# Performance work log

Measured on AMD Instinct MI355X. Metric: run time of the kernel, lower is better.

## Reference

```python
import jax, jax.numpy as jnp
import numpy as np

N = 32768       # batch of states
DQ = 8          # q_ndim (dof_ndim)
A = 4           # action_dim
H = 1024        # hidden_size


def setup_inputs() -> dict:
    key = jax.random.key(0)
    ks = jax.random.split(key, 16)

    def lin(kw, kb, fan_out, fan_in, zero_bias=False):
        s = 1.0 / np.sqrt(fan_in)
        W = jax.random.normal(kw, (fan_out, fan_in), dtype=jnp.float32) * s
        b = jnp.zeros((fan_out,), jnp.float32) if zero_bias else \
            jax.random.normal(kb, (fan_out,), dtype=jnp.float32) * s
        return W, b

    W1, b1 = lin(ks[0], ks[1], H, 2 * DQ)            # h_net layer 1
    W2, b2 = lin(ks[2], ks[3], H, H)                 # h_net layer 2
    Wh, bh = lin(ks[4], ks[5], 1, H)                 # h_net head -> scalar H(z)
    Wf1, bf1 = lin(ks[6], ks[7], H, 2 * DQ + A)      # flex_net layer 1
    Wf2, bf2 = lin(ks[8], ks[9], H, H)               # flex_net layer 2
    Wff, bff = lin(ks[10], ks[11], 2 * DQ, H)        # flex_net head -> 2*q_ndim
    Wp, bp = lin(ks[12], ks[13], A, 2 * DQ)          # control policy (detached)

    return {
        "t": jnp.zeros((), jnp.float32),
        "z": jax.random.normal(ks[14], (N, 2 * DQ), dtype=jnp.float32),
        "W1": W1, "b1": b1, "W2": W2, "b2": b2, "Wh": Wh, "bh": bh,
        "Wf1": Wf1, "bf1": bf1, "Wf2": Wf2, "bf2": bf2, "Wff": Wff, "bff": bff,
        "Wp": Wp, "bp": bp,
    }


def reference(t, z, W1, b1, W2, b2, Wh, bh,
              Wf1, bf1, Wf2, bf2, Wff, bff, Wp, bp):
    # control input, detached as in the torch forward (u = policy(t, z).detach())
    u = jax.lax.stop_gradient(jnp.tanh(z @ Wp.T + bp))  # [N, A]

    # ---- H-net forward, saving tanh' at each activation (the `sps` list) ----
    # angular_dims=() -> CosSin is the identity, so h_net[0](z) = z.
    a1 = z @ W1.T + b1          # [N, H]
    h1 = jnp.tanh(a1)
    s0 = 1.0 - h1 * h1          # d tanh / d a1   (sps[0])
    a2 = h1 @ W2.T + b2         # [N, H]
    h2 = jnp.tanh(a2)
    s1 = 1.0 - h2 * h2          # d tanh / d a2   (sps[1])

    # dH = grad_z sum(h_net(z)), with gradients flowing (create_graph=True)
    def H_sum(zz):
        hh = jnp.tanh(zz @ W1.T + b1)
        hh = jnp.tanh(hh @ W2.T + b2)
        return jnp.sum(hh @ Wh.T + bh)

    dH = jax.grad(H_sum)(z)     # [N, 2*DQ]

    # ---- flex-net with skip term modulated by reversed tanh' maps ----
    zu = jnp.concatenate([z, u], axis=-1)       # [N, 2*DQ + A]
    f1 = zu @ Wf1.T + bf1
    g1 = jnp.tanh(f1) + f1 * s1                 # idx = 1 -> sps[1]
    f2 = g1 @ Wf2.T + bf2
    g2 = jnp.tanh(f2) + f2 * s0                 # idx = 0 -> sps[0]
    out = g2 @ Wff.T + bff                      # [N, 2*DQ]

    # D = jacobian of CosSin = identity per batch row (angular_dims=()), so
    # bmm(out[:,None,:], D).squeeze(1) == out.

    # dz_dt = J @ (out + dH):  J([top; bot]) = [bot; -top]
    s = out + dH
    return jnp.concatenate([s[:, DQ:], -s[:, :DQ]], axis=-1)  # [N, 2*DQ]
```

## Files before the change

kernel.cpp:

```cpp
#include <hip/hip_runtime.h>
#include <hip/hip_bf16.h>

typedef __hip_bfloat16 bf16;
typedef __attribute__((ext_vector_type(8))) short short8;
typedef __attribute__((ext_vector_type(4))) short s16x4;
typedef __attribute__((ext_vector_type(4))) float f32x4;

__device__ __forceinline__ bf16 f2b(float f) { return __float2bfloat16(f); }
__device__ __forceinline__ short bfbits(float f) {
  union { float f; unsigned u; } x; x.f = f;
  unsigned r = x.u + 0x7fff + ((x.u >> 16) & 1);
  return (short)(r >> 16);
}
__device__ __forceinline__ float tanh_fast(float x) {
  float t = __expf(-2.f * fabsf(x));
  float r = (1.f - t) * __builtin_amdgcn_rcpf(1.f + t);
  return copysignf(r, x);
}

#define GLOAD_LDS16(gp, lp) __builtin_amdgcn_global_load_lds( \
    (const __attribute__((address_space(1))) void*)(gp), \
    (__attribute__((address_space(3))) void*)(lp), 16, 0, 0)
#define SBAR() __builtin_amdgcn_s_barrier()
#define WAITV(n) do { asm volatile("s_waitcnt vmcnt(" #n ")" ::: "memory"); \
                      __builtin_amdgcn_sched_barrier(0); } while (0)

__global__ __launch_bounds__(256) void prep(
    const float* __restrict__ W2, const float* __restrict__ Wf2,
    const float* __restrict__ W1, const float* __restrict__ Wff,
    bf16* __restrict__ W2bf, bf16* __restrict__ W2Tbf,
    bf16* __restrict__ Wf2bf, bf16* __restrict__ W1n,
    bf16* __restrict__ Wffn)
{
  __shared__ float T[32][33];
  const int tid = threadIdx.x, bx = blockIdx.x;
  const int tx = bx & 31, ty = bx >> 5;
  const int r = tid >> 3, c4 = (tid & 7) * 4;
  const long ibase = (long)(ty * 32 + r) * 1024 + tx * 32 + c4;

  f32x4 v = *(const f32x4*)(W2 + ibase);
  f32x4 vf = *(const f32x4*)(Wf2 + ibase);
  s16x4 sv, sf;
  #pragma unroll
  for (int j = 0; j < 4; ++j) {
    sv[j] = bfbits(v[j]); sf[j] = bfbits(vf[j]);
    T[r][c4 + j] = v[j];
  }
  *(s16x4*)(W2bf + ibase) = sv;
  *(s16x4*)(Wf2bf + ibase) = sf;
  __syncthreads();
  const int oc = tid >> 3, or4 = (tid & 7) * 4;
  s16x4 st;
  #pragma unroll
  for (int j = 0; j < 4; ++j) st[j] = bfbits(T[or4 + j][oc]);
  *(s16x4*)(W2Tbf + (long)(tx * 32 + oc) * 1024 + ty * 32 + or4) = st;

  if (bx < 32) {
    #pragma unroll
    for (int rep = 0; rep < 2; ++rep) {
      int i = bx * 512 + rep * 256 + tid;
      int rr = i >> 10, cc = i & 1023;
      W1n[i] = f2b(W1[cc * 16 + rr]);
      Wffn[i] = f2b(Wff[i]);
    }
  }
}

__global__ __launch_bounds__(256) void k1(
    const float* __restrict__ z, const float* __restrict__ W1,
    const float* __restrict__ b1, const float* __restrict__ Wp,
    const float* __restrict__ bp, const float* __restrict__ Wf1,
    const float* __restrict__ bf1v,
    bf16* __restrict__ h1, bf16* __restrict__ f1out, long grow0)
{
  __shared__ float zs[32][16];
  __shared__ float us[32][4];
  const int tid = threadIdx.x;
  const long r0 = (long)blockIdx.x * 32;
  for (int i = tid; i < 512; i += 256) {
    int r = i >> 4, c = i & 15;
    zs[r][c] = z[(grow0 + r0 + r) * 16 + c];
  }
  __syncthreads();
  if (tid < 128) {
    int r = tid >> 2, a = tid & 3;
    float acc = bp[a];
    #pragma unroll
    for (int k = 0; k < 16; ++k) acc = fmaf(zs[r][k], Wp[a * 16 + k], acc);
    us[r][a] = tanh_fast(acc);
  }
  __syncthreads();
  #pragma unroll
  for (int jj = 0; jj < 4; ++jj) {
    const int c = tid + jj * 256;
    {
      float w[16];
      #pragma unroll
      for (int k = 0; k < 16; ++k) w[k] = W1[c * 16 + k];
      const float bc = b1[c];
      for (int r = 0; r < 32; ++r) {
        float a = bc;
        #pragma unroll
        for (int k = 0; k < 16; ++k) a = fmaf(zs[r][k], w[k], a);
        h1[(r0 + r) * 1024 + c] = f2b(tanh_fast(a));
      }
    }
    {
      float wf[20];
      #pragma unroll
      for (int k = 0; k < 20; ++k) wf[k] = Wf1[c * 20 + k];
      const float bfc = bf1v[c];
      for (int r = 0; r < 32; ++r) {
        float f = bfc;
        #pragma unroll
        for (int k = 0; k < 16; ++k) f = fmaf(zs[r][k], wf[k], f);
        #pragma unroll
        for (int a = 0; a < 4; ++a) f = fmaf(us[r][a], wf[16 + a], f);
        f1out[(r0 + r) * 1024 + c] = f2b(f);
      }
    }
  }
}

__global__ __launch_bounds__(512, 2) void gemm0(
    const bf16* __restrict__ A, const bf16* __restrict__ Bp,
    const float* __restrict__ bias, const float* __restrict__ Whv,
    bf16* O1, bf16* __restrict__ O2)
{
  __shared__ __align__(16) char smem[131072];
  const int tid = threadIdx.x;
  const int lane = tid & 63, wid = tid >> 6;
  const int wr = wid >> 2, wc = wid & 3;
  const int fr = lane & 15, kg = lane >> 4;
  const long row0 = (long)blockIdx.x * 256;
  const int col0 = blockIdx.y * 256;

  const int sr0 = tid >> 2;
  const int sk0 = ((tid & 3) ^ ((tid >> 3) & 3)) * 8;
  const int swr = (fr >> 1) & 3;

  const bf16* gA0 = A + (row0 + sr0) * 1024 + sk0;
  const bf16* gB0 = Bp + ((long)col0 + sr0) * 1024 + sk0;
  const int rdA = (wr * 128 + fr) * 32 + (kg ^ swr) * 8;
  const int rdB = (wc * 64 + fr) * 32 + (kg ^ swr) * 8;

  f32x4 acc[8][4] = {};

  auto stage = [&](int b, int k0) {
    bf16* as = (bf16*)smem + b * 8192;
    bf16* bs = (bf16*)smem + 32768 + b * 8192;
    GLOAD_LDS16(gA0 + k0, as + tid * 8);
    GLOAD_LDS16(gA0 + 128 * 1024 + k0, as + 4096 + tid * 8);
    GLOAD_LDS16(gB0 + k0, bs + tid * 8);
    GLOAD_LDS16(gB0 + 128 * 1024 + k0, bs + 4096 + tid * 8);
  };

  stage(0, 0); stage(1, 32); stage(2, 64);
  WAITV(8); SBAR();

  #pragma unroll
  for (int kt = 0; kt < 32; ++kt) {
    if (kt + 3 < 32) stage((kt + 3) & 3, (kt + 3) * 32);
    const bf16* as = (const bf16*)smem + (kt & 3) * 8192;
    const bf16* bs = (const bf16*)smem + 32768 + (kt & 3) * 8192;
    short8 af[8], bfr[4];
    #pragma unroll
    for (int m = 0; m < 8; ++m)
      af[m] = *(const short8*)(as + rdA + m * 512);
    #pragma unroll
    for (int n = 0; n < 4; ++n)
      bfr[n] = *(const short8*)(bs + rdB + n * 512);
    __builtin_amdgcn_s_setprio(1);
    #pragma unroll
    for (int m = 0; m < 8; ++m)
      #pragma unroll
      for (int n = 0; n < 4; ++n)
        acc[m][n] = __builtin_amdgcn_mfma_f32_16x16x32_bf16(af[m], bfr[n], acc[m][n], 0, 0, 0);
    __builtin_amdgcn_s_setprio(0);
    if (kt < 29)       WAITV(8);
    else if (kt == 29) WAITV(4);
    else if (kt == 30) WAITV(0);
    if (kt < 31) SBAR();
  }

  #pragma unroll
  for (int m = 0; m < 8; ++m) {
    const long gr0 = row0 + wr * 128 + m * 16 + kg * 4;
    #pragma unroll
    for (int n = 0; n < 4; ++n) {
      const int gc = col0 + wc * 64 + n * 16 + fr;
      const float b2c = bias[gc], whc = Whv[gc];
      f32x4 v = acc[m][n];
      #pragma unroll
      for (int j = 0; j < 4; ++j) {
        const long idx = (gr0 + j) * 1024 + gc;
        float h = tanh_fast(v[j] + b2c);
        float s1v = 1.f - h * h;
        float f = __bfloat162float(((const bf16*)O1)[idx]);
        O2[idx] = f2b(s1v * whc);
        O1[idx] = f2b(tanh_fast(f) + f * s1v);
      }
    }
  }
}

__global__ __launch_bounds__(256, 2) void gemm12(
    const bf16* __restrict__ Ab, const bf16* __restrict__ Af,
    const bf16* __restrict__ Bw, const bf16* __restrict__ Bf,
    const float* __restrict__ bf2v, const bf16* __restrict__ h1,
    const bf16* __restrict__ W1n, const bf16* __restrict__ Wffn,
    float* __restrict__ Pp, int ckRows)
{
  __shared__ __align__(16) char smem[65536];
  const int tid = threadIdx.x;
  const int lane = tid & 63, wid = tid >> 6;
  const int wr = wid >> 1, wc = wid & 1;
  const int fr = lane & 15, kg = lane >> 4;

  const int q = (int)gridDim.x >> 3;
  const int wgid = ((int)blockIdx.x & 7) * q + ((int)blockIdx.x >> 3);
  const long row0 = (long)(wgid >> 3) * 128;
  const int col0 = (wgid & 7) * 128;
  const int cb = wgid & 7;

  const int sr0 = tid >> 2;
  const int sk0 = ((tid & 3) ^ ((tid >> 3) & 3)) * 8;
  const int swr = (fr >> 1) & 3;

  const bf16* gAb = Ab + (row0 + sr0) * 1024 + sk0;
  const bf16* gAf = Af + (row0 + sr0) * 1024 + sk0;
  const bf16* gBw = Bw + ((long)col0 + sr0) * 1024 + sk0;
  const bf16* gBf = Bf + ((long)col0 + sr0) * 1024 + sk0;
  const int rdA = (wr * 64 + fr) * 32 + (kg ^ swr) * 8;
  const int rdB = (wc * 64 + fr) * 32 + (kg ^ swr) * 8;

  f32x4 accB[4][4] = {}, accF[4][4] = {};

  auto stage = [&](int b, int k0) {
    bf16* s = (bf16*)smem + b * 16384;
    GLOAD_LDS16(gAb + k0, s + tid * 8);
    GLOAD_LDS16(gAb + 64 * 1024 + k0, s + 2048 + tid * 8);
    GLOAD_LDS16(gAf + k0, s + 4096 + tid * 8);
    GLOAD_LDS16(gAf + 64 * 1024 + k0, s + 6144 + tid * 8);
    GLOAD_LDS16(gBw + k0, s + 8192 + tid * 8);
    GLOAD_LDS16(gBw + 64 * 1024 + k0, s + 10240 + tid * 8);
    GLOAD_LDS16(gBf + k0, s + 12288 + tid * 8);
    GLOAD_LDS16(gBf + 64 * 1024 + k0, s + 14336 + tid * 8);
  };

  stage(0, 0);
  __syncthreads();

  #pragma unroll 2
  for (int kt = 0; kt < 32; ++kt) {
    const int cur = kt & 1;
    if (kt < 31) stage(cur ^ 1, (kt + 1) * 32);
    const bf16* s = (const bf16*)smem + cur * 16384;
    short8 afB[4], afF[4], bfW[4], bfFr[4];
    #pragma unroll
    for (int m = 0; m < 4; ++m) {
      afB[m] = *(const short8*)(s + rdA + m * 512);
      afF[m] = *(const short8*)(s + 4096 + rdA + m * 512);
    }
    #pragma unroll
    for (int n = 0; n < 4; ++n) {
      bfW[n]  = *(const short8*)(s + 8192 + rdB + n * 512);
      bfFr[n] = *(const short8*)(s + 12288 + rdB + n * 512);
    }
    __builtin_amdgcn_s_setprio(1);
    #pragma unroll
    for (int m = 0; m < 4; ++m)
      #pragma unroll
      for (int n = 0; n < 4; ++n) {
        accB[m][n] = __builtin_amdgcn_mfma_f32_16x16x32_bf16(afB[m], bfW[n], accB[m][n], 0, 0, 0);
        accF[m][n] = __builtin_amdgcn_mfma_f32_16x16x32_bf16(afF[m], bfFr[n], accF[m][n], 0, 0, 0);
      }
    __builtin_amdgcn_s_setprio(0);
    __syncthreads();
  }

  bf16* Ot = (bf16*)smem;
  f32x4 pacc[2] = {};
  #pragma unroll
  for (int m = 0; m < 4; ++m) {
    const int rl0 = wr * 64 + m * 16 + kg * 4;
    const long gr0 = row0 + rl0;
    #pragma unroll
    for (int n = 0; n < 4; ++n) {
      const int cl = wc * 64 + n * 16 + fr;
      const int gc = col0 + cl;
      f32x4 v = accB[m][n];
      #pragma unroll
      for (int j = 0; j < 4; ++j) {
        const long idx = (gr0 + j) * 1024 + gc;
        float hh = __bfloat162float(h1[idx]);
        Ot[(rl0 + j) * 136 + cl] = f2b(v[j] * (1.f - hh * hh));
      }
    }
  }
  __syncthreads();
  #pragma unroll
  for (int sub = 0; sub < 2; ++sub) {
    const int rl0 = wid * 32 + sub * 16;
    #pragma unroll
    for (int ks = 0; ks < 4; ++ks) {
      short8 afrag = *(const short8*)(Ot + (rl0 + fr) * 136 + ks * 32 + kg * 8);
      short8 bfrag = *(const short8*)(W1n + fr * 1024 + col0 + ks * 32 + kg * 8);
      pacc[sub] = __builtin_amdgcn_mfma_f32_16x16x32_bf16(afrag, bfrag, pacc[sub], 0, 0, 0);
    }
  }
  __syncthreads();
  #pragma unroll
  for (int m = 0; m < 4; ++m) {
    const int rl0 = wr * 64 + m * 16 + kg * 4;
    const long gr0 = row0 + rl0;
    #pragma unroll
    for (int n = 0; n < 4; ++n) {
      const int cl = wc * 64 + n * 16 + fr;
      const int gc = col0 + cl;
      const float bfc = bf2v[gc];
      f32x4 v = accF[m][n];
      #pragma unroll
      for (int j = 0; j < 4; ++j) {
        const long idx = (gr0 + j) * 1024 + gc;
        float hh = __bfloat162float(h1[idx]);
        float f = v[j] + bfc;
        Ot[(rl0 + j) * 136 + cl] = f2b(tanh_fast(f) + f * (1.f - hh * hh));
      }
    }
  }
  __syncthreads();
  #pragma unroll
  for (int sub = 0; sub < 2; ++sub) {
    const int rl0 = wid * 32 + sub * 16;
    #pragma unroll
    for (int ks = 0; ks < 4; ++ks) {
      short8 afrag = *(const short8*)(Ot + (rl0 + fr) * 136 + ks * 32 + kg * 8);
      short8 bfrag = *(const short8*)(Wffn + fr * 1024 + col0 + ks * 32 + kg * 8);
      pacc[sub] = __builtin_amdgcn_mfma_f32_16x16x32_bf16(afrag, bfrag, pacc[sub], 0, 0, 0);
    }
    #pragma unroll
    for (int j = 0; j < 4; ++j)
      Pp[(((long)cb) * ckRows + row0 + rl0 + kg * 4 + j) * 16 + fr] = pacc[sub][j];
  }
}

__global__ __launch_bounds__(256) void k7(
    const float* __restrict__ Pp, const float* __restrict__ bff,
    float* __restrict__ out, long grow0, int ckRows)
{
  int i = blockIdx.x * 256 + threadIdx.x;
  int r = i >> 4, j = i & 15, jp = (j + 8) & 15;
  float s = bff[jp];
  #pragma unroll
  for (int cb = 0; cb < 8; ++cb)
    s += Pp[((long)cb * ckRows + r) * 16 + jp];
  out[(grow0 + r) * 16 + j] = (j < 8) ? s : -s;
}

extern "C" void kernel_launch(void* const* d_in, const int* in_sizes, int n_in,
                              void* d_out, int out_size, void* d_ws, size_t ws_size,
                              hipStream_t stream) {
  const float* z   = (const float*)d_in[1];
  const float* W1  = (const float*)d_in[2];
  const float* b1  = (const float*)d_in[3];
  const float* W2  = (const float*)d_in[4];
  const float* b2  = (const float*)d_in[5];
  const float* Wh  = (const float*)d_in[6];
  const float* Wf1 = (const float*)d_in[8];
  const float* bf1 = (const float*)d_in[9];
  const float* Wf2 = (const float*)d_in[10];
  const float* bf2 = (const float*)d_in[11];
  const float* Wff = (const float*)d_in[12];
  const float* bff = (const float*)d_in[13];
  const float* Wp  = (const float*)d_in[14];
  const float* bp  = (const float*)d_in[15];
  float* out = (float*)d_out;
  const int N = in_sizes[1] / 16;

  char* p = (char*)d_ws;
  auto alloc = [&](size_t bytes) {
    char* q = p; p += (bytes + 255) & ~(size_t)255; return q;
  };
  bf16* W2bf  = (bf16*)alloc(1024 * 1024 * 2);
  bf16* W2Tbf = (bf16*)alloc(1024 * 1024 * 2);
  bf16* Wf2bf = (bf16*)alloc(1024 * 1024 * 2);
  bf16* W1n   = (bf16*)alloc(16 * 1024 * 2);
  bf16* Wffn  = (bf16*)alloc(16 * 1024 * 2);
  size_t wbytes = (size_t)(p - (char*)d_ws);

  int CK = N;
  while (CK > 256 && wbytes + (size_t)CK * 6656 > ws_size) CK >>= 1;
  bf16* actA = (bf16*)alloc((size_t)CK * 2048);
  bf16* actB = (bf16*)alloc((size_t)CK * 2048);
  bf16* actD = (bf16*)alloc((size_t)CK * 2048);
  float* Pp  = (float*)alloc((size_t)CK * 8 * 16 * 4);

  prep<<<1024, 256, 0, stream>>>(W2, Wf2, W1, Wff, W2bf, W2Tbf, Wf2bf, W1n, Wffn);

  for (long r0 = 0; r0 < N; r0 += CK) {
    k1<<<CK / 32, 256, 0, stream>>>(z, W1, b1, Wp, bp, Wf1, bf1, actA, actD, r0);
    gemm0<<<dim3(CK / 256, 4), 512, 0, stream>>>(
        actA, W2bf, b2, Wh, actD, actB);
    gemm12<<<(CK / 128) * 8, 256, 0, stream>>>(
        actB, actD, W2Tbf, Wf2bf, bf2, actA, W1n, Wffn, Pp, CK);
    k7<<<CK / 16, 256, 0, stream>>>(Pp, bff, out, r0, CK);
  }
}
```

Measured before the change: 355.6 us.

## Use 512-thread blocks and triple-buffered LDS pipeline in gemm12

The dual GEMM kernel moves from 4 to 8 waves per block, each owning a 64x32 sub-tile, and from double to triple buffering of the LDS K-tiles. Barriers are replaced by explicit vmcnt waits so two tiles stay in flight. This is meant to hide global-load latency and raise the number of waves per block. In exchange it uses 96KB of LDS and one block per CU, so occupancy drops from two blocks of four waves per CU.

Measured after the change: 381.4 us. 1.07x slower.

```diff
diff --git a/kernel.cpp b/kernel.cpp
--- a/kernel.cpp
+++ b/kernel.cpp
@@ -204,17 +204,17 @@
   }
 }
 
-__global__ __launch_bounds__(256, 2) void gemm12(
+__global__ __launch_bounds__(512, 1) void gemm12(
     const bf16* __restrict__ Ab, const bf16* __restrict__ Af,
     const bf16* __restrict__ Bw, const bf16* __restrict__ Bf,
     const float* __restrict__ bf2v, const bf16* __restrict__ h1,
     const bf16* __restrict__ W1n, const bf16* __restrict__ Wffn,
     float* __restrict__ Pp, int ckRows)
 {
-  __shared__ __align__(16) char smem[65536];
+  __shared__ __align__(16) char smem[98304];
   const int tid = threadIdx.x;
   const int lane = tid & 63, wid = tid >> 6;
-  const int wr = wid >> 1, wc = wid & 1;
+  const int wr = wid >> 2, wc = wid & 3;
   const int fr = lane & 15, kg = lane >> 4;
 
   const int q = (int)gridDim.x >> 3;
@@ -232,38 +232,33 @@
   const bf16* gBw = Bw + ((long)col0 + sr0) * 1024 + sk0;
   const bf16* gBf = Bf + ((long)col0 + sr0) * 1024 + sk0;
   const int rdA = (wr * 64 + fr) * 32 + (kg ^ swr) * 8;
-  const int rdB = (wc * 64 + fr) * 32 + (kg ^ swr) * 8;
-
-  f32x4 accB[4][4] = {}, accF[4][4] = {};
+  const int rdB = (wc * 32 + fr) * 32 + (kg ^ swr) * 8;
+
+  f32x4 accB[4][2] = {}, accF[4][2] = {};
 
   auto stage = [&](int b, int k0) {
     bf16* s = (bf16*)smem + b * 16384;
     GLOAD_LDS16(gAb + k0, s + tid * 8);
-    GLOAD_LDS16(gAb + 64 * 1024 + k0, s + 2048 + tid * 8);
     GLOAD_LDS16(gAf + k0, s + 4096 + tid * 8);
-    GLOAD_LDS16(gAf + 64 * 1024 + k0, s + 6144 + tid * 8);
     GLOAD_LDS16(gBw + k0, s + 8192 + tid * 8);
-    GLOAD_LDS16(gBw + 64 * 1024 + k0, s + 10240 + tid * 8);
     GLOAD_LDS16(gBf + k0, s + 12288 + tid * 8);
-    GLOAD_LDS16(gBf + 64 * 1024 + k0, s + 14336 + tid * 8);
   };
 
-  stage(0, 0);
-  __syncthreads();
-
-  #pragma unroll 2
+  stage(0, 0); stage(1, 32);
+  WAITV(4); SBAR();
+
+  #pragma unroll
   for (int kt = 0; kt < 32; ++kt) {
-    const int cur = kt & 1;
-    if (kt < 31) stage(cur ^ 1, (kt + 1) * 32);
-    const bf16* s = (const bf16*)smem + cur * 16384;
-    short8 afB[4], afF[4], bfW[4], bfFr[4];
+    if (kt + 2 < 32) stage((kt + 2) % 3, (kt + 2) * 32);
+    const bf16* s = (const bf16*)smem + (kt % 3) * 16384;
+    short8 afB[4], afF[4], bfW[2], bfFr[2];
     #pragma unroll
     for (int m = 0; m < 4; ++m) {
       afB[m] = *(const short8*)(s + rdA + m * 512);
       afF[m] = *(const short8*)(s + 4096 + rdA + m * 512);
     }
     #pragma unroll
-    for (int n = 0; n < 4; ++n) {
+    for (int n = 0; n < 2; ++n) {
       bfW[n]  = *(const short8*)(s + 8192 + rdB + n * 512);
       bfFr[n] = *(const short8*)(s + 12288 + rdB + n * 512);
     }
@@ -271,23 +266,26 @@
     #pragma unroll
     for (int m = 0; m < 4; ++m)
       #pragma unroll
-      for (int n = 0; n < 4; ++n) {
+      for (int n = 0; n < 2; ++n) {
         accB[m][n] = __builtin_amdgcn_mfma_f32_16x16x32_bf16(afB[m], bfW[n], accB[m][n], 0, 0, 0);
         accF[m][n] = __builtin_amdgcn_mfma_f32_16x16x32_bf16(afF[m], bfFr[n], accF[m][n], 0, 0, 0);
       }
     __builtin_amdgcn_s_setprio(0);
-    __syncthreads();
-  }
-
+    if (kt < 30)       WAITV(4);
+    else if (kt == 30) WAITV(0);
+    if (kt < 31) SBAR();
+  }
+
+  __syncthreads();
   bf16* Ot = (bf16*)smem;
-  f32x4 pacc[2] = {};
+  f32x4 pacc = (f32x4){0.f, 0.f, 0.f, 0.f};
   #pragma unroll
   for (int m = 0; m < 4; ++m) {
     const int rl0 = wr * 64 + m * 16 + kg * 4;
     const long gr0 = row0 + rl0;
     #pragma unroll
-    for (int n = 0; n < 4; ++n) {
-      const int cl = wc * 64 + n * 16 + fr;
+    for (int n = 0; n < 2; ++n) {
+      const int cl = wc * 32 + n * 16 + fr;
       const int gc = col0 + cl;
       f32x4 v = accB[m][n];
       #pragma unroll
@@ -299,14 +297,13 @@
     }
   }
   __syncthreads();
-  #pragma unroll
-  for (int sub = 0; sub < 2; ++sub) {
-    const int rl0 = wid * 32 + sub * 16;
+  {
+    const int rl0 = wid * 16;
     #pragma unroll
     for (int ks = 0; ks < 4; ++ks) {
       short8 afrag = *(const short8*)(Ot + (rl0 + fr) * 136 + ks * 32 + kg * 8);
       short8 bfrag = *(const short8*)(W1n + fr * 1024 + col0 + ks * 32 + kg * 8);
-      pacc[sub] = __builtin_amdgcn_mfma_f32_16x16x32_bf16(afrag, bfrag, pacc[sub], 0, 0, 0);
+      pacc = __builtin_amdgcn_mfma_f32_16x16x32_bf16(afrag, bfrag, pacc, 0, 0, 0);
     }
   }
   __syncthreads();
@@ -315,8 +312,8 @@
     const int rl0 = wr * 64 + m * 16 + kg * 4;
     const long gr0 = row0 + rl0;
     #pragma unroll
-    for (int n = 0; n < 4; ++n) {
-      const int cl = wc * 64 + n * 16 + fr;
+    for (int n = 0; n < 2; ++n) {
+      const int cl = wc * 32 + n * 16 + fr;
       const int gc = col0 + cl;
       const float bfc = bf2v[gc];
       f32x4 v = accF[m][n];
@@ -330,18 +327,17 @@
     }
   }
   __syncthreads();
-  #pragma unroll
-  for (int sub = 0; sub < 2; ++sub) {
-    const int rl0 = wid * 32 + sub * 16;
+  {
+    const int rl0 = wid * 16;
     #pragma unroll
     for (int ks = 0; ks < 4; ++ks) {
       short8 afrag = *(const short8*)(Ot + (rl0 + fr) * 136 + ks * 32 + kg * 8);
       short8 bfrag = *(const short8*)(Wffn + fr * 1024 + col0 + ks * 32 + kg * 8);
-      pacc[sub] = __builtin_amdgcn_mfma_f32_16x16x32_bf16(afrag, bfrag, pacc[sub], 0, 0, 0);
+      pacc = __builtin_amdgcn_mfma_f32_16x16x32_bf16(afrag, bfrag, pacc, 0, 0, 0);
     }
     #pragma unroll
     for (int j = 0; j < 4; ++j)
-      Pp[(((long)cb) * ckRows + row0 + rl0 + kg * 4 + j) * 16 + fr] = pacc[sub][j];
+      Pp[(((long)cb) * ckRows + row0 + rl0 + kg * 4 + j) * 16 + fr] = pacc[j];
   }
 }
 
@@ -402,7 +398,7 @@
     k1<<<CK / 32, 256, 0, stream>>>(z, W1, b1, Wp, bp, Wf1, bf1, actA, actD, r0);
     gemm0<<<dim3(CK / 256, 4), 512, 0, stream>>>(
         actA, W2bf, b2, Wh, actD, actB);
-    gemm12<<<(CK / 128) * 8, 256, 0, stream>>>(
+    gemm12<<<(CK / 128) * 8, 512, 0, stream>>>(
         actB, actD, W2Tbf, Wf2bf, bf2, actA, W1n, Wffn, Pp, CK);
     k7<<<CK / 16, 256, 0, stream>>>(Pp, bff, out, r0, CK);
   }
```
